# Kernel optimization log

Hardware: AMD Instinct MI355X
Metric: run time of the kernel (lower is better)

## Reference

```python
import jax, jax.numpy as jnp
import numpy as np

MARGIN = 0.5
POS_WEIGHT = 0.5
NEG_WEIGHT = 0.5
PUNISHMENT_SCALE = 2.0
POS_THRESHOLD = 0.6
NEG_THRESHOLD = 0.3
BIG = 1e9  # finite sentinel instead of inf (grad-safe under where)


def setup_inputs() -> dict:
    key = jax.random.key(0)
    k1, k2, k3 = jax.random.split(key, 3)
    N, D = 8192, 256
    embeddings = jax.random.normal(k1, (N, D), dtype=jnp.float32)
    labels = jax.random.randint(k2, (N,), 0, 2, dtype=jnp.int32)
    pids = jax.random.randint(k3, (N,), 0, 256, dtype=jnp.int32)
    return {"embeddings": embeddings, "labels": labels, "pids": pids}


def reference(embeddings, labels, pids):
    N = embeddings.shape[0]
    # F.normalize(p=2, dim=1): x / max(||x||, eps)
    norm = jnp.maximum(jnp.linalg.norm(embeddings, axis=1, keepdims=True), 1e-12)
    normed = embeddings / norm
    sim = normed @ normed.T  # (N, N) cosine similarity

    same_pid = pids[:, None] == pids[None, :]            # (N, N)
    genuine_j = (labels == 1)[None, :]                   # (1, N)
    not_self = ~jnp.eye(N, dtype=bool)
    pos_mask = same_pid & genuine_j & not_self           # same pid, genuine, not anchor
    neg_mask = (same_pid & ~genuine_j) | ~same_pid       # same-pid forgeries or cross-pid

    valid = (labels == 1) & pos_mask.any(axis=1) & neg_mask.any(axis=1)

    # hardest positive = min similarity among positives
    hp = jnp.min(jnp.where(pos_mask, sim, BIG), axis=1)  # (N,)

    # semi-hard negatives: hp - margin < sim < hp
    semi = neg_mask & (sim < hp[:, None]) & (sim > (hp - MARGIN)[:, None])
    cand = neg_mask & (sim > hp[:, None])                # harder-than-positive negatives
    hn_semi = jnp.max(jnp.where(semi, sim, -BIG), axis=1)
    hn_cand = jnp.max(jnp.where(cand, sim, -BIG), axis=1)
    hn_all = jnp.max(jnp.where(neg_mask, sim, -BIG), axis=1)
    hn = jnp.where(semi.any(axis=1), hn_semi,
                   jnp.where(cand.any(axis=1), hn_cand, hn_all))

    base = jax.nn.relu(hn - hp + MARGIN)
    weight = jnp.where((hp < POS_THRESHOLD) | (hn > NEG_THRESHOLD),
                       PUNISHMENT_SCALE, 1.0)
    loss = base * weight + POS_WEIGHT * (1.0 - hp) + NEG_WEIGHT * jax.nn.relu(hn + 0.2)

    cnt = jnp.sum(valid)
    total = jnp.sum(jnp.where(valid, loss, 0.0))
    return jnp.where(cnt > 0, total / jnp.maximum(cnt, 1), 0.0)
```

## Files before the change

kernel.cpp:

```cpp
#include <hip/hip_runtime.h>
#include <hip/hip_bf16.h>
#include <stdint.h>

typedef __attribute__((ext_vector_type(8))) short short8;
typedef __attribute__((ext_vector_type(4))) float f32x4;

#define BIGF 1e9f
#define NSLOT 64
#define MAXM 96

__device__ inline float blo(unsigned int u) {
    union { unsigned int i; float f; } v; v.i = u << 16; return v.f;
}
__device__ inline float bhi(unsigned int u) {
    union { unsigned int i; float f; } v; v.i = u & 0xffff0000u; return v.f;
}
__device__ inline unsigned int fkey(float s) {
    unsigned int b = __float_as_uint(s);
    return (b & 0x80000000u) ? ~b : (b | 0x80000000u);
}
__device__ inline float funkey(unsigned int k) {
    unsigned int b = (k & 0x80000000u) ? (k & 0x7fffffffu) : ~k;
    return __uint_as_float(b);
}
__device__ inline void async16(const unsigned short* g, unsigned short* l) {
    __builtin_amdgcn_global_load_lds(
        (const __attribute__((address_space(1))) void*)g,
        (__attribute__((address_space(3))) void*)l, 16, 0, 0);
}
__device__ inline unsigned short f2b(float x) {
    __hip_bfloat16 h = __float2bfloat16(x);
    return *reinterpret_cast<unsigned short*>(&h);
}

__global__ __launch_bounds__(256) void k_normalize(
    const float* __restrict__ emb, const int* __restrict__ labels,
    const int* __restrict__ pids, unsigned short* __restrict__ normed,
    int* __restrict__ gpid, float* __restrict__ hp_init,
    float* __restrict__ gred, int* __restrict__ done)
{
    if (blockIdx.x == 0 && threadIdx.x < 3) {
        if (threadIdx.x < 2) gred[threadIdx.x] = 0.f;
        else *done = 0;
    }
    int w = threadIdx.x >> 6, lane = threadIdx.x & 63;
    int row = blockIdx.x * 4 + w;
    const float4* src = (const float4*)(emb + ((size_t)row << 8));
    float4 x = src[lane];
    float ss = x.x * x.x + x.y * x.y + x.z * x.z + x.w * x.w;
    #pragma unroll
    for (int off = 32; off >= 1; off >>= 1) ss += __shfl_xor(ss, off, 64);
    float inv = 1.0f / fmaxf(sqrtf(ss), 1e-12f);
    ushort4 o;
    o.x = f2b(x.x * inv); o.y = f2b(x.y * inv);
    o.z = f2b(x.z * inv); o.w = f2b(x.w * inv);
    ((ushort4*)(normed + ((size_t)row << 8)))[lane] = o;
    if (lane == 0) {
        gpid[row] = (labels[row] == 1) ? pids[row] : -1;
        hp_init[row] = BIGF;
    }
}

__global__ __launch_bounds__(256) void k_hp_pid(
    const unsigned short* __restrict__ normed, const int* __restrict__ labels,
    const int* __restrict__ pids, float* __restrict__ hp_out, int N, int D)
{
    __shared__ int list[MAXM];
    __shared__ unsigned int hp_loc[MAXM];
    __shared__ unsigned short rows[MAXM * 256];
    __shared__ int cnt;
    int p = blockIdx.x;
    int t = threadIdx.x;
    if (t == 0) cnt = 0;
    __syncthreads();
    for (int j = t; j < N; j += 256)
        if (pids[j] == p && labels[j] == 1) {
            int idx = atomicAdd(&cnt, 1);
            if (idx < MAXM) list[idx] = j;
        }
    __syncthreads();
    int M = min(cnt, MAXM);
    for (int s = t; s < M; s += 256) hp_loc[s] = 0xFFFFFFFFu;
    for (int idx = t; idx < M * 32; idx += 256) {
        int mi = idx >> 5, ch = idx & 31;
        ((uint4*)&rows[mi * 256])[ch] =
            ((const uint4*)(normed + ((size_t)list[mi] << 8)))[ch];
    }
    __syncthreads();
    for (int pr = t; pr < M * M; pr += 256) {
        int i = pr / M, j = pr - i * M;
        if (i == j) continue;
        const uint4* ap = (const uint4*)&rows[i * 256];
        const uint4* bp = (const uint4*)&rows[j * 256];
        float s = 0.f;
        #pragma unroll 4
        for (int k = 0; k < 32; ++k) {
            uint4 a = ap[k], b = bp[k];
            s += blo(a.x) * blo(b.x) + bhi(a.x) * bhi(b.x);
            s += blo(a.y) * blo(b.y) + bhi(a.y) * bhi(b.y);
            s += blo(a.z) * blo(b.z) + bhi(a.z) * bhi(b.z);
            s += blo(a.w) * blo(b.w) + bhi(a.w) * bhi(b.w);
        }
        atomicMin(&hp_loc[i], fkey(s));
    }
    __syncthreads();
    for (int s = t; s < M; s += 256) {
        unsigned int key = hp_loc[s];
        hp_out[list[s]] = (key == 0xFFFFFFFFu) ? BIGF : funkey(key);
    }
}

__global__ __launch_bounds__(256) void k_pass2(
    const unsigned short* __restrict__ normed, const int* __restrict__ pids,
    const int* __restrict__ gpid, const float* __restrict__ hp,
    float* __restrict__ p_hnall, float* __restrict__ p_mbel, int N)
{
    const int b = blockIdx.x;
    int rt = (int)floorf((129.0f - sqrtf(16641.0f - 8.0f * (float)b)) * 0.5f);
    rt = min(rt, 63);
    while (64 * (rt + 1) - ((rt + 1) * rt) / 2 <= b) ++rt;
    while (64 * rt - (rt * (rt - 1)) / 2 > b) --rt;
    const int ct = rt + (b - (64 * rt - (rt * (rt - 1)) / 2));
    const bool diag = (ct == rt);

    __shared__ unsigned short As[2][128 * 32];
    __shared__ unsigned short Bs[2][128 * 32];
    __shared__ float hp_r[128], hp_c[128];
    __shared__ int pid_r[128], gpid_r[128], pid_c[128], gpid_c[128];
    __shared__ unsigned int red1[128], red2[128], red3[128], red4[128];

    const int t = threadIdx.x;
    const int lane = t & 63;
    const int w = t >> 6;
    const int wr = w & 1, wc = w >> 1;
    const int quad = lane >> 4, l16 = lane & 15;
    const int rbase = rt * 128, cbase = ct * 128;

    if (t < 128) {
        hp_r[t] = hp[rbase + t];
        pid_r[t] = pids[rbase + t];
        gpid_r[t] = gpid[rbase + t];
        hp_c[t] = hp[cbase + t];
        pid_c[t] = pids[cbase + t];
        gpid_c[t] = gpid[cbase + t];
        red1[t] = 0u; red2[t] = 0u; red3[t] = 0u; red4[t] = 0u;
    }

    const int r0 = t >> 2, p0 = t & 3;
    const int c0 = p0 ^ ((r0 >> 1) & 3);
    const unsigned short* gA0 = normed + ((size_t)(rbase + r0) << 8) + c0 * 8;
    const unsigned short* gA1 = normed + ((size_t)(rbase + r0 + 64) << 8) + c0 * 8;
    const unsigned short* gB0 = normed + ((size_t)(cbase + r0) << 8) + c0 * 8;
    const unsigned short* gB1 = normed + ((size_t)(cbase + r0 + 64) << 8) + c0 * 8;

    async16(gA0, &As[0][t * 8]);
    async16(gA1, &As[0][2048 + t * 8]);
    if (!diag) {
        async16(gB0, &Bs[0][t * 8]);
        async16(gB1, &Bs[0][2048 + t * 8]);
    }

    f32x4 acc[4][4];
    #pragma unroll
    for (int mt = 0; mt < 4; ++mt)
        #pragma unroll
        for (int nt = 0; nt < 4; ++nt)
            acc[mt][nt] = (f32x4){0.f, 0.f, 0.f, 0.f};

    const int sw = (l16 >> 1) & 3;
    const int aoff = (wr * 64 + l16) * 32 + (quad ^ sw) * 8;
    const int boff = (wc * 64 + l16) * 32 + (quad ^ sw) * 8;

    const unsigned short* Bbase[2] = { diag ? &As[0][0] : &Bs[0][0],
                                       diag ? &As[1][0] : &Bs[1][0] };

    for (int kb = 0; kb < 8; ++kb) {
        __syncthreads();
        int cur = kb & 1;
        if (kb < 7) {
            int nxt = cur ^ 1;
            int ko = (kb + 1) << 5;
            async16(gA0 + ko, &As[nxt][t * 8]);
            async16(gA1 + ko, &As[nxt][2048 + t * 8]);
            if (!diag) {
                async16(gB0 + ko, &Bs[nxt][t * 8]);
                async16(gB1 + ko, &Bs[nxt][2048 + t * 8]);
            }
        }
        short8 af[4], bf[4];
        #pragma unroll
        for (int mt = 0; mt < 4; ++mt)
            af[mt] = *reinterpret_cast<const short8*>(&As[cur][aoff + mt * 512]);
        #pragma unroll
        for (int nt = 0; nt < 4; ++nt)
            bf[nt] = *reinterpret_cast<const short8*>(&Bbase[cur][boff + nt * 512]);
        #pragma unroll
        for (int mt = 0; mt < 4; ++mt)
            #pragma unroll
            for (int nt = 0; nt < 4; ++nt)
                acc[mt][nt] = __builtin_amdgcn_mfma_f32_16x16x32_bf16(
                    af[mt], bf[nt], acc[mt][nt], 0, 0, 0);
    }

    int gp[4];
    #pragma unroll
    for (int nt = 0; nt < 4; ++nt) gp[nt] = gpid_c[wc * 64 + nt * 16 + l16];
    #pragma unroll
    for (int mt = 0; mt < 4; ++mt) {
        #pragma unroll
        for (int r = 0; r < 4; ++r) {
            int rl = wr * 64 + mt * 16 + quad * 4 + r;
            int prow = pid_r[rl];
            float hprow = hp_r[rl];
            float v1 = -BIGF, v2 = -BIGF;
            #pragma unroll
            for (int nt = 0; nt < 4; ++nt) {
                float s = acc[mt][nt][r];
                float tt = (prow != gp[nt]) ? s : -BIGF;
                v1 = fmaxf(v1, tt);
                float t2 = (tt < hprow) ? tt : -BIGF;
                v2 = fmaxf(v2, t2);
            }
            #pragma unroll
            for (int off = 8; off >= 1; off >>= 1) {
                v1 = fmaxf(v1, __shfl_xor(v1, off, 64));
                v2 = fmaxf(v2, __shfl_xor(v2, off, 64));
            }
            if (l16 == 0) {
                atomicMax(&red1[rl], fkey(v1));
                atomicMax(&red2[rl], fkey(v2));
            }
        }
    }

    if (!diag) {
        int4 gr[4];
        #pragma unroll
        for (int mt = 0; mt < 4; ++mt)
            gr[mt] = *(const int4*)&gpid_r[wr * 64 + mt * 16 + quad * 4];
        #pragma unroll
        for (int nt = 0; nt < 4; ++nt) {
            int c = wc * 64 + nt * 16 + l16;
            int pc = pid_c[c];
            float hpc = hp_c[c];
            float v1 = -BIGF, v2 = -BIGF;
            #pragma unroll
            for (int mt = 0; mt < 4; ++mt) {
                const int* g = (const int*)&gr[mt];
                #pragma unroll
                for (int r = 0; r < 4; ++r) {
                    float s = acc[mt][nt][r];
                    float tt = (pc != g[r]) ? s : -BIGF;
                    v1 = fmaxf(v1, tt);
                    float t2 = (tt < hpc) ? tt : -BIGF;
                    v2 = fmaxf(v2, t2);
                }
            }
            v1 = fmaxf(v1, __shfl_xor(v1, 16, 64));
            v1 = fmaxf(v1, __shfl_xor(v1, 32, 64));
            v2 = fmaxf(v2, __shfl_xor(v2, 16, 64));
            v2 = fmaxf(v2, __shfl_xor(v2, 32, 64));
            if (quad == 0) {
                atomicMax(&red3[c], fkey(v1));
                atomicMax(&red4[c], fkey(v2));
            }
        }
    }

    __syncthreads();
    if (t < 128) {
        p_hnall[(size_t)ct * N + rbase + t] = funkey(red1[t]);
        p_mbel[(size_t)ct * N + rbase + t] = funkey(red2[t]);
        if (!diag) {
            p_hnall[(size_t)rt * N + cbase + t] = funkey(red3[t]);
            p_mbel[(size_t)rt * N + cbase + t] = funkey(red4[t]);
        }
    }
}

__global__ __launch_bounds__(256) void k_rowloss(
    const float* __restrict__ hp, const float* __restrict__ p_hnall,
    const float* __restrict__ p_mbel, const int* __restrict__ labels,
    float* __restrict__ gred, int* __restrict__ done,
    float* __restrict__ out, int N)
{
    int i = blockIdx.x * 256 + threadIdx.x;
    float hn_all = -BIGF, mb = -BIGF;
    #pragma unroll 8
    for (int s = 0; s < NSLOT; ++s) {
        hn_all = fmaxf(hn_all, p_hnall[(size_t)s * N + i]);
        mb = fmaxf(mb, p_mbel[(size_t)s * N + i]);
    }
    float hpv = hp[i];
    bool valid = (labels[i] == 1) && (hpv < 1e8f) && (hn_all > -1e8f);
    float hn = (mb > hpv - 0.5f) ? mb : hn_all;
    float base = fmaxf(hn - hpv + 0.5f, 0.f);
    float wgt = (hpv < 0.6f || hn > 0.3f) ? 2.f : 1.f;
    float loss = base * wgt + 0.5f * (1.f - hpv) + 0.5f * fmaxf(hn + 0.2f, 0.f);
    float lsum = valid ? loss : 0.f;
    float lcnt = valid ? 1.f : 0.f;
    #pragma unroll
    for (int off = 32; off >= 1; off >>= 1) {
        lsum += __shfl_xor(lsum, off, 64);
        lcnt += __shfl_xor(lcnt, off, 64);
    }
    __shared__ float rs[4], rc[4];
    int wv = threadIdx.x >> 6, lane = threadIdx.x & 63;
    if (lane == 0) { rs[wv] = lsum; rc[wv] = lcnt; }
    __syncthreads();
    if (threadIdx.x == 0) {
        atomicAdd(&gred[0], rs[0] + rs[1] + rs[2] + rs[3]);
        atomicAdd(&gred[1], rc[0] + rc[1] + rc[2] + rc[3]);
        __threadfence();
        int old = atomicAdd(done, 1);
        if (old == (int)gridDim.x - 1) {
            float S = atomicAdd(&gred[0], 0.f);
            float C = atomicAdd(&gred[1], 0.f);
            out[0] = (C > 0.f) ? S / fmaxf(C, 1.f) : 0.f;
        }
    }
}

extern "C" void kernel_launch(void* const* d_in, const int* in_sizes, int n_in,
                              void* d_out, int out_size, void* d_ws, size_t ws_size,
                              hipStream_t stream)
{
    const float* emb = (const float*)d_in[0];
    const int* labels = (const int*)d_in[1];
    const int* pids = (const int*)d_in[2];
    float* out = (float*)d_out;
    int N = in_sizes[1];
    int D = in_sizes[0] / N;

    char* ws = (char*)d_ws;
    unsigned short* normed = (unsigned short*)ws;  ws += (size_t)N * D * 2;
    int* gpid = (int*)ws;                          ws += (size_t)N * 4;
    float* hp = (float*)ws;                        ws += (size_t)N * 4;
    float* p_hnall = (float*)ws;                   ws += (size_t)N * NSLOT * 4;
    float* p_mbel = (float*)ws;                    ws += (size_t)N * NSLOT * 4;
    float* gred = (float*)ws;                      ws += 2 * 4;
    int* done = (int*)ws;                          ws += 4;

    int M = N / 128;
    int tri = M * (M + 1) / 2;

    k_normalize<<<N / 4, 256, 0, stream>>>(emb, labels, pids, normed, gpid, hp,
                                           gred, done);
    k_hp_pid<<<256, 256, 0, stream>>>(normed, labels, pids, hp, N, D);
    k_pass2<<<tri, 256, 0, stream>>>(normed, pids, gpid, hp,
                                     p_hnall, p_mbel, N);
    k_rowloss<<<N / 256, 256, 0, stream>>>(hp, p_hnall, p_mbel, labels,
                                           gred, done, out, N);
}
```

Before: 149.8 us.

## Single-buffer LDS tiles, pack pid/genuine ids, and raise pass2 occupancy

```diff
diff --git a/kernel.cpp b/kernel.cpp
--- a/kernel.cpp
+++ b/kernel.cpp
@@ -36,7 +36,7 @@
 __global__ __launch_bounds__(256) void k_normalize(
     const float* __restrict__ emb, const int* __restrict__ labels,
     const int* __restrict__ pids, unsigned short* __restrict__ normed,
-    int* __restrict__ gpid, float* __restrict__ hp_init,
+    int* __restrict__ pg, float* __restrict__ hp_init,
     float* __restrict__ gred, int* __restrict__ done)
 {
     if (blockIdx.x == 0 && threadIdx.x < 3) {
@@ -56,7 +56,8 @@
     o.z = f2b(x.z * inv); o.w = f2b(x.w * inv);
     ((ushort4*)(normed + ((size_t)row << 8)))[lane] = o;
     if (lane == 0) {
-        gpid[row] = (labels[row] == 1) ? pids[row] : -1;
+        int g = (labels[row] == 1) ? pids[row] : -1;
+        pg[row] = (pids[row] & 0xffff) | ((g + 1) << 16);
         hp_init[row] = BIGF;
     }
 }
@@ -110,9 +111,9 @@
     }
 }
 
-__global__ __launch_bounds__(256) void k_pass2(
-    const unsigned short* __restrict__ normed, const int* __restrict__ pids,
-    const int* __restrict__ gpid, const float* __restrict__ hp,
+__global__ __launch_bounds__(256, 5) void k_pass2(
+    const unsigned short* __restrict__ normed, const int* __restrict__ pg,
+    const float* __restrict__ hp,
     float* __restrict__ p_hnall, float* __restrict__ p_mbel, int N)
 {
     const int b = blockIdx.x;
@@ -123,10 +124,10 @@
     const int ct = rt + (b - (64 * rt - (rt * (rt - 1)) / 2));
     const bool diag = (ct == rt);
 
-    __shared__ unsigned short As[2][128 * 32];
-    __shared__ unsigned short Bs[2][128 * 32];
+    __shared__ unsigned short As[128 * 32];
+    __shared__ unsigned short Bs[128 * 32];
     __shared__ float hp_r[128], hp_c[128];
-    __shared__ int pid_r[128], gpid_r[128], pid_c[128], gpid_c[128];
+    __shared__ int pg_r[128], pg_c[128];
     __shared__ unsigned int red1[128], red2[128], red3[128], red4[128];
 
     const int t = threadIdx.x;
@@ -138,11 +139,9 @@
 
     if (t < 128) {
         hp_r[t] = hp[rbase + t];
-        pid_r[t] = pids[rbase + t];
-        gpid_r[t] = gpid[rbase + t];
+        pg_r[t] = pg[rbase + t];
         hp_c[t] = hp[cbase + t];
-        pid_c[t] = pids[cbase + t];
-        gpid_c[t] = gpid[cbase + t];
+        pg_c[t] = pg[cbase + t];
         red1[t] = 0u; red2[t] = 0u; red3[t] = 0u; red4[t] = 0u;
     }
 
@@ -153,11 +152,11 @@
     const unsigned short* gB0 = normed + ((size_t)(cbase + r0) << 8) + c0 * 8;
     const unsigned short* gB1 = normed + ((size_t)(cbase + r0 + 64) << 8) + c0 * 8;
 
-    async16(gA0, &As[0][t * 8]);
-    async16(gA1, &As[0][2048 + t * 8]);
+    async16(gA0, &As[t * 8]);
+    async16(gA1, &As[2048 + t * 8]);
     if (!diag) {
-        async16(gB0, &Bs[0][t * 8]);
-        async16(gB1, &Bs[0][2048 + t * 8]);
+        async16(gB0, &Bs[t * 8]);
+        async16(gB1, &Bs[2048 + t * 8]);
     }
 
     f32x4 acc[4][4];
@@ -170,99 +169,99 @@
     const int sw = (l16 >> 1) & 3;
     const int aoff = (wr * 64 + l16) * 32 + (quad ^ sw) * 8;
     const int boff = (wc * 64 + l16) * 32 + (quad ^ sw) * 8;
-
-    const unsigned short* Bbase[2] = { diag ? &As[0][0] : &Bs[0][0],
-                                       diag ? &As[1][0] : &Bs[1][0] };
+    const unsigned short* Bb = diag ? As : Bs;
+
+    __syncthreads();
 
     for (int kb = 0; kb < 8; ++kb) {
+        short8 af[4], bf[4];
+        #pragma unroll
+        for (int mt = 0; mt < 4; ++mt)
+            af[mt] = *reinterpret_cast<const short8*>(&As[aoff + mt * 512]);
+        #pragma unroll
+        for (int nt = 0; nt < 4; ++nt)
+            bf[nt] = *reinterpret_cast<const short8*>(&Bb[boff + nt * 512]);
         __syncthreads();
-        int cur = kb & 1;
         if (kb < 7) {
-            int nxt = cur ^ 1;
             int ko = (kb + 1) << 5;
-            async16(gA0 + ko, &As[nxt][t * 8]);
-            async16(gA1 + ko, &As[nxt][2048 + t * 8]);
+            async16(gA0 + ko, &As[t * 8]);
+            async16(gA1 + ko, &As[2048 + t * 8]);
             if (!diag) {
-                async16(gB0 + ko, &Bs[nxt][t * 8]);
-                async16(gB1 + ko, &Bs[nxt][2048 + t * 8]);
+                async16(gB0 + ko, &Bs[t * 8]);
+                async16(gB1 + ko, &Bs[2048 + t * 8]);
             }
         }
-        short8 af[4], bf[4];
-        #pragma unroll
-        for (int mt = 0; mt < 4; ++mt)
-            af[mt] = *reinterpret_cast<const short8*>(&As[cur][aoff + mt * 512]);
-        #pragma unroll
-        for (int nt = 0; nt < 4; ++nt)
-            bf[nt] = *reinterpret_cast<const short8*>(&Bbase[cur][boff + nt * 512]);
         #pragma unroll
         for (int mt = 0; mt < 4; ++mt)
             #pragma unroll
             for (int nt = 0; nt < 4; ++nt)
                 acc[mt][nt] = __builtin_amdgcn_mfma_f32_16x16x32_bf16(
                     af[mt], bf[nt], acc[mt][nt], 0, 0, 0);
-    }
-
-    int gp[4];
-    #pragma unroll
-    for (int nt = 0; nt < 4; ++nt) gp[nt] = gpid_c[wc * 64 + nt * 16 + l16];
-    #pragma unroll
-    for (int mt = 0; mt < 4; ++mt) {
-        #pragma unroll
-        for (int r = 0; r < 4; ++r) {
-            int rl = wr * 64 + mt * 16 + quad * 4 + r;
-            int prow = pid_r[rl];
-            float hprow = hp_r[rl];
-            float v1 = -BIGF, v2 = -BIGF;
+        __syncthreads();
+    }
+
+    {
+        const unsigned int gcH0 = ((unsigned int)pg_c[wc * 64 +  0 + l16]) >> 16;
+        const unsigned int gcH1 = ((unsigned int)pg_c[wc * 64 + 16 + l16]) >> 16;
+        const unsigned int gcH2 = ((unsigned int)pg_c[wc * 64 + 32 + l16]) >> 16;
+        const unsigned int gcH3 = ((unsigned int)pg_c[wc * 64 + 48 + l16]) >> 16;
+        #pragma unroll
+        for (int mt = 0; mt < 4; ++mt) {
             #pragma unroll
-            for (int nt = 0; nt < 4; ++nt) {
-                float s = acc[mt][nt][r];
-                float tt = (prow != gp[nt]) ? s : -BIGF;
-                v1 = fmaxf(v1, tt);
-                float t2 = (tt < hprow) ? tt : -BIGF;
-                v2 = fmaxf(v2, t2);
+            for (int r = 0; r < 4; ++r) {
+                const int rl = wr * 64 + mt * 16 + quad * 4 + r;
+                const unsigned int prP1 = ((unsigned int)pg_r[rl] & 0xffffu) + 1u;
+                const float hprow = hp_r[rl];
+                float tt0 = (prP1 != gcH0) ? acc[mt][0][r] : -BIGF;
+                float tt1 = (prP1 != gcH1) ? acc[mt][1][r] : -BIGF;
+                float tt2 = (prP1 != gcH2) ? acc[mt][2][r] : -BIGF;
+                float tt3 = (prP1 != gcH3) ? acc[mt][3][r] : -BIGF;
+                float v1 = fmaxf(fmaxf(tt0, tt1), fmaxf(tt2, tt3));
+                float u0 = (tt0 < hprow) ? tt0 : -BIGF;
+                float u1 = (tt1 < hprow) ? tt1 : -BIGF;
+                float u2 = (tt2 < hprow) ? tt2 : -BIGF;
+                float u3 = (tt3 < hprow) ? tt3 : -BIGF;
+                float v2 = fmaxf(fmaxf(u0, u1), fmaxf(u2, u3));
+                v1 = fmaxf(v1, __shfl_xor(v1, 8, 64));
+                v2 = fmaxf(v2, __shfl_xor(v2, 8, 64));
+                v1 = fmaxf(v1, __shfl_xor(v1, 4, 64));
+                v2 = fmaxf(v2, __shfl_xor(v2, 4, 64));
+                if (l16 < 4) {
+                    atomicMax(&red1[rl], fkey(v1));
+                    atomicMax(&red2[rl], fkey(v2));
+                }
             }
-            #pragma unroll
-            for (int off = 8; off >= 1; off >>= 1) {
-                v1 = fmaxf(v1, __shfl_xor(v1, off, 64));
-                v2 = fmaxf(v2, __shfl_xor(v2, off, 64));
-            }
-            if (l16 == 0) {
-                atomicMax(&red1[rl], fkey(v1));
-                atomicMax(&red2[rl], fkey(v2));
-            }
         }
     }
 
     if (!diag) {
-        int4 gr[4];
-        #pragma unroll
-        for (int mt = 0; mt < 4; ++mt)
-            gr[mt] = *(const int4*)&gpid_r[wr * 64 + mt * 16 + quad * 4];
         #pragma unroll
         for (int nt = 0; nt < 4; ++nt) {
-            int c = wc * 64 + nt * 16 + l16;
-            int pc = pid_c[c];
-            float hpc = hp_c[c];
-            float v1 = -BIGF, v2 = -BIGF;
+            const int c = wc * 64 + nt * 16 + l16;
+            const unsigned int pcP1 = ((unsigned int)pg_c[c] & 0xffffu) + 1u;
+            const float hpc = hp_c[c];
+            float a1 = -BIGF, b1 = -BIGF;
             #pragma unroll
             for (int mt = 0; mt < 4; ++mt) {
-                const int* g = (const int*)&gr[mt];
-                #pragma unroll
-                for (int r = 0; r < 4; ++r) {
-                    float s = acc[mt][nt][r];
-                    float tt = (pc != g[r]) ? s : -BIGF;
-                    v1 = fmaxf(v1, tt);
-                    float t2 = (tt < hpc) ? tt : -BIGF;
-                    v2 = fmaxf(v2, t2);
-                }
+                const int4 pr4 = *(const int4*)&pg_r[wr * 64 + mt * 16 + quad * 4];
+                float tt0 = (pcP1 != (((unsigned int)pr4.x) >> 16)) ? acc[mt][nt][0] : -BIGF;
+                float tt1 = (pcP1 != (((unsigned int)pr4.y) >> 16)) ? acc[mt][nt][1] : -BIGF;
+                float tt2 = (pcP1 != (((unsigned int)pr4.z) >> 16)) ? acc[mt][nt][2] : -BIGF;
+                float tt3 = (pcP1 != (((unsigned int)pr4.w) >> 16)) ? acc[mt][nt][3] : -BIGF;
+                a1 = fmaxf(a1, fmaxf(fmaxf(tt0, tt1), fmaxf(tt2, tt3)));
+                float u0 = (tt0 < hpc) ? tt0 : -BIGF;
+                float u1 = (tt1 < hpc) ? tt1 : -BIGF;
+                float u2 = (tt2 < hpc) ? tt2 : -BIGF;
+                float u3 = (tt3 < hpc) ? tt3 : -BIGF;
+                b1 = fmaxf(b1, fmaxf(fmaxf(u0, u1), fmaxf(u2, u3)));
             }
-            v1 = fmaxf(v1, __shfl_xor(v1, 16, 64));
-            v1 = fmaxf(v1, __shfl_xor(v1, 32, 64));
-            v2 = fmaxf(v2, __shfl_xor(v2, 16, 64));
-            v2 = fmaxf(v2, __shfl_xor(v2, 32, 64));
+            a1 = fmaxf(a1, __shfl_xor(a1, 16, 64));
+            b1 = fmaxf(b1, __shfl_xor(b1, 16, 64));
+            a1 = fmaxf(a1, __shfl_xor(a1, 32, 64));
+            b1 = fmaxf(b1, __shfl_xor(b1, 32, 64));
             if (quad == 0) {
-                atomicMax(&red3[c], fkey(v1));
-                atomicMax(&red4[c], fkey(v2));
+                atomicMax(&red3[c], fkey(a1));
+                atomicMax(&red4[c], fkey(b1));
             }
         }
     }
@@ -334,7 +333,7 @@
 
     char* ws = (char*)d_ws;
     unsigned short* normed = (unsigned short*)ws;  ws += (size_t)N * D * 2;
-    int* gpid = (int*)ws;                          ws += (size_t)N * 4;
+    int* pg = (int*)ws;                            ws += (size_t)N * 4;
     float* hp = (float*)ws;                        ws += (size_t)N * 4;
     float* p_hnall = (float*)ws;                   ws += (size_t)N * NSLOT * 4;
     float* p_mbel = (float*)ws;                    ws += (size_t)N * NSLOT * 4;
@@ -344,11 +343,10 @@
     int M = N / 128;
     int tri = M * (M + 1) / 2;
 
-    k_normalize<<<N / 4, 256, 0, stream>>>(emb, labels, pids, normed, gpid, hp,
+    k_normalize<<<N / 4, 256, 0, stream>>>(emb, labels, pids, normed, pg, hp,
                                            gred, done);
     k_hp_pid<<<256, 256, 0, stream>>>(normed, labels, pids, hp, N, D);
-    k_pass2<<<tri, 256, 0, stream>>>(normed, pids, gpid, hp,
-                                     p_hnall, p_mbel, N);
+    k_pass2<<<tri, 256, 0, stream>>>(normed, pg, hp, p_hnall, p_mbel, N);
     k_rowloss<<<N / 256, 256, 0, stream>>>(hp, p_hnall, p_mbel, labels,
                                            gred, done, out, N);
 }
```

Result: slower. 211.1 us (+40.9%).
